# Kernel tuning notes

Hardware: AMD Instinct MI355X
Metric: run time of the kernel (lower is better)

## Reference

```python
import jax, jax.numpy as jnp
import numpy as np

N = 100000      # nodes
E = 3200000     # edges
F_IN = 78       # num_features_mol
F_GAT = 256     # mol_out_feats
HEADS = 2
F_HYP = 128     # mol_out_feats_hyper


def setup_inputs() -> dict:
    key = jax.random.key(0)
    ks = jax.random.split(key, 32)
    g = lambda k, s: jax.random.normal(k, s, dtype=jnp.float32) * 0.05
    inp = {}
    inp["mol_x"] = jax.random.normal(ks[0], (N, F_IN), dtype=jnp.float32)
    inp["mol_edge_index"] = jax.random.randint(ks[1], (2, E), 0, N)
    inp["hyper_edge"] = jax.random.randint(ks[2], (2, E), 0, N)
    # GAT layer 1 (78 -> 256, 2 heads, concat=False)
    inp["W1"] = g(ks[3], (F_IN, HEADS * F_GAT)); inp["as1"] = g(ks[4], (HEADS, F_GAT)); inp["ad1"] = g(ks[5], (HEADS, F_GAT)); inp["b1"] = jnp.zeros((F_GAT,), jnp.float32)
    # GAT layers 2,3 (256 -> 256)
    inp["W2"] = g(ks[6], (F_GAT, HEADS * F_GAT)); inp["as2"] = g(ks[7], (HEADS, F_GAT)); inp["ad2"] = g(ks[8], (HEADS, F_GAT)); inp["b2"] = jnp.zeros((F_GAT,), jnp.float32)
    inp["W3"] = g(ks[9], (F_GAT, HEADS * F_GAT)); inp["as3"] = g(ks[10], (HEADS, F_GAT)); inp["ad3"] = g(ks[11], (HEADS, F_GAT)); inp["b3"] = jnp.zeros((F_GAT,), jnp.float32)
    # GRU-style gating fusion
    inp["fc1_w"] = g(ks[12], (F_GAT, F_GAT)); inp["fc1_b"] = jnp.zeros((F_GAT,), jnp.float32)
    inp["fc2_w"] = g(ks[13], (F_GAT, F_GAT)); inp["fc2_b"] = jnp.zeros((F_GAT,), jnp.float32)
    inp["mol_bias"] = jax.random.uniform(ks[14], (1, F_GAT), jnp.float32, -0.2, 0.2)
    # HypergraphConv layers (334 -> 128 -> 128)
    inp["theta1"] = g(ks[15], (F_GAT + F_IN, F_HYP)); inp["hb1"] = jnp.zeros((F_HYP,), jnp.float32)
    inp["theta2"] = g(ks[16], (F_HYP, F_HYP)); inp["hb2"] = jnp.zeros((F_HYP,), jnp.float32)
    return inp


def _gat(x, src, dst, W, a_s, a_d, b):
    # PyG GATConv, heads=2, concat=False, eval mode (no dropout), self-loops pre-added in src/dst
    xh = (x @ W).reshape(N, HEADS, F_GAT)            # [N,H,C]
    a_src = (xh * a_s).sum(-1)                        # [N,H]
    a_dst = (xh * a_d).sum(-1)                        # [N,H]
    e = jax.nn.leaky_relu(a_src[src] + a_dst[dst], 0.2)  # [E',H]
    m = jax.ops.segment_max(e, dst, num_segments=N)
    ex = jnp.exp(e - m[dst])
    s = jax.ops.segment_sum(ex, dst, num_segments=N)
    alpha = ex / s[dst]                               # softmax over incoming edges
    out = jax.ops.segment_sum(xh[src] * alpha[:, :, None], dst, num_segments=N)
    return out.mean(axis=1) + b                       # concat=False -> head mean


def _hyper(x, node, edge, theta, b):
    # PyG HypergraphConv, use_attention=False: D^-1 H B^-1 H^T X Theta + b
    xt = x @ theta
    ones = jnp.ones((node.shape[0],), xt.dtype)
    D = jax.ops.segment_sum(ones, node, num_segments=N)
    B = jax.ops.segment_sum(ones, edge, num_segments=N)
    Dinv = jnp.where(D > 0, 1.0 / D, 0.0)
    Binv = jnp.where(B > 0, 1.0 / B, 0.0)
    ef = Binv[:, None] * jax.ops.segment_sum(xt[node], edge, num_segments=N)
    nf = Dinv[:, None] * jax.ops.segment_sum(ef[edge], node, num_segments=N)
    return nf + b


def _forward(mol_x, mol_edge_index, hyper_edge,
             W1, as1, ad1, b1, W2, as2, ad2, b2, W3, as3, ad3, b3,
             fc1_w, fc1_b, fc2_w, fc2_b, mol_bias, theta1, hb1, theta2, hb2):
    loops = jnp.arange(N, dtype=mol_edge_index.dtype)
    src = jnp.concatenate([mol_edge_index[0], loops])
    dst = jnp.concatenate([mol_edge_index[1], loops])
    hyper_x0 = jax.lax.stop_gradient(mol_x)  # .clone().detach()
    # layer 0
    h = jax.nn.relu(_gat(mol_x, src, dst, W1, as1, ad1, b1))
    # layer 1 (relu) + gate
    x = jax.nn.relu(_gat(h, src, dst, W2, as2, ad2, b2))
    z = jax.nn.sigmoid(x @ fc1_w.T + fc1_b + h @ fc2_w.T + fc2_b + mol_bias)
    h = z * x + (1.0 - z) * h
    # layer 2 (no relu) + gate
    x = _gat(h, src, dst, W3, as3, ad3, b3)
    z = jax.nn.sigmoid(x @ fc1_w.T + fc1_b + h @ fc2_w.T + fc2_b + mol_bias)
    h = z * x + (1.0 - z) * h
    # hypergraph branch (source uses mol_edge_index here, hyper_edge is unused)
    hx = jnp.concatenate([jax.lax.stop_gradient(h), hyper_x0], axis=1)
    node, edge = mol_edge_index[0], mol_edge_index[1]
    hx = jax.nn.relu(_hyper(hx, node, edge, theta1, hb1))
    hx = jax.nn.relu(_hyper(hx, node, edge, theta2, hb2))
    return jnp.concatenate([h, hx], axis=1)  # [N, 384]


def reference(mol_x, mol_edge_index, hyper_edge,
              W1, as1, ad1, b1, W2, as2, ad2, b2, W3, as3, ad3, b3,
              fc1_w, fc1_b, fc2_w, fc2_b, mol_bias, theta1, hb1, theta2, hb2):
    return _forward(mol_x, mol_edge_index, hyper_edge,
                    W1, as1, ad1, b1, W2, as2, ad2, b2, W3, as3, ad3, b3,
                    fc1_w, fc1_b, fc2_w, fc2_b, mol_bias, theta1, hb1, theta2, hb2)
```

## Files before the change

### kernel.cpp

```cpp
#include <hip/hip_runtime.h>

typedef unsigned short u16;
typedef __attribute__((ext_vector_type(8))) short short8v;
typedef __attribute__((ext_vector_type(8))) unsigned short ushort8v;
typedef __attribute__((ext_vector_type(4))) unsigned short ushort4v;
typedef __attribute__((ext_vector_type(4))) float f32x4;
typedef __attribute__((ext_vector_type(2))) float f32x2;

__device__ __forceinline__ float bf2f(u16 u) {
    union { unsigned int i; float f; } v; v.i = ((unsigned int)u) << 16; return v.f;
}
__device__ __forceinline__ u16 f2bf(float f) {
    union { float f; unsigned int i; } v; v.f = f;
    unsigned int i = v.i;
    return (u16)((i + 0x7FFFu + ((i >> 16) & 1u)) >> 16);
}
__device__ __forceinline__ float leaky02(float x) { return x > 0.f ? x : 0.2f * x; }
__device__ __forceinline__ float load_in(const void* p, long i, int isbf) {
    return isbf ? bf2f(((const u16*)p)[i]) : ((const float*)p)[i];
}
__device__ __forceinline__ f32x2 pk_fma(f32x2 a, f32x2 b, f32x2 c) {
    f32x2 d;
    asm("v_pk_fma_f32 %0, %1, %2, %3" : "=v"(d) : "v"(a), "v"(b), "v"(c));
    return d;
}
__device__ __forceinline__ f32x2 pk_add(f32x2 a, f32x2 b) {
    f32x2 d;
    asm("v_pk_add_f32 %0, %1, %2" : "=v"(d) : "v"(a), "v"(b));
    return d;
}
__device__ __forceinline__ f32x2 bfpair(unsigned int d) {
    union { unsigned int i; float f; } lo, hi;
    lo.i = d << 16;
    hi.i = d & 0xFFFF0000u;
    f32x2 r; r.x = lo.f; r.y = hi.f; return r;
}
#define GLD_LDS16(g, s) __builtin_amdgcn_global_load_lds( \
    (const __attribute__((address_space(1))) void*)(g),   \
    (__attribute__((address_space(3))) void*)(s), 16, 0, 0)

__global__ void detect_kernel(const unsigned* __restrict__ w, int* __restrict__ flag) {
    __shared__ int cnt;
    int t = threadIdx.x;
    if (t == 0) cnt = 0;
    __syncthreads();
    unsigned x = w[t * 16];
    unsigned lo = x & 0xFFFFu;
    int e = (int)((x >> 7) & 0xFFu);
    int good = (lo == 0u) || (e >= 100 && e <= 140);
    atomicAdd(&cnt, good);
    __syncthreads();
    if (t == 0) *flag = (cnt > 128) ? 1 : 0;
}

#define CSR_NBK 1024

__global__ __launch_bounds__(256)
void bucket_count_kernel(const int* __restrict__ ei, int* __restrict__ bcs,
                         int* __restrict__ bcd, int E_, int n, int SH) {
    __shared__ int hs[CSR_NBK], hd[CSR_NBK];
    const int t = threadIdx.x;
    for (int i = t; i < CSR_NBK; i += 256) { hs[i] = 0; hd[i] = 0; }
    __syncthreads();
    const int e0 = blockIdx.x * 4096;
    #pragma unroll
    for (int k = 0; k < 16; ++k) {
        int e = e0 + k * 256 + t;
        if (e < E_) {
            int s = ei[e], d = ei[E_ + e];
            if ((unsigned)s >= (unsigned)n) s = 0;
            if ((unsigned)d >= (unsigned)n) d = 0;
            atomicAdd(&hs[s >> SH], 1);
            atomicAdd(&hd[d >> SH], 1);
        }
    }
    __syncthreads();
    for (int i = t; i < CSR_NBK; i += 256) {
        if (hs[i]) atomicAdd(&bcs[i], hs[i]);
        if (hd[i]) atomicAdd(&bcd[i], hd[i]);
    }
}

__global__ void scan_excl_kernel(const int* __restrict__ deg, int* __restrict__ ptr, int n) {
    __shared__ int s_woff[17];
    __shared__ int s_carry;
    const int t = threadIdx.x;
    const int lane = t & 63, wid = t >> 6;
    if (t == 0) s_carry = 0;
    __syncthreads();
    for (int base = 0; base < n; base += 1024) {
        int i = base + t;
        int v = (i < n) ? deg[i] : 0;
        int incl = v;
        #pragma unroll
        for (int d = 1; d < 64; d <<= 1) {
            int x = __shfl_up(incl, d, 64);
            if (lane >= d) incl += x;
        }
        if (lane == 63) s_woff[wid] = incl;
        __syncthreads();
        if (t == 0) {
            int run = 0;
            #pragma unroll
            for (int w = 0; w < 16; ++w) { int x = s_woff[w]; s_woff[w] = run; run += x; }
            s_woff[16] = run;
        }
        __syncthreads();
        int excl = s_carry + s_woff[wid] + incl - v;
        if (i < n) ptr[i] = excl;
        __syncthreads();
        if (t == 0) s_carry += s_woff[16];
        __syncthreads();
    }
    if (t == 0) ptr[n] = s_carry;
}

__global__ void copy2_kernel(const int* __restrict__ a, int* __restrict__ b,
                             const int* __restrict__ c, int* __restrict__ d2, int n) {
    int i = blockIdx.x * 256 + threadIdx.x;
    if (i < n) { b[i] = a[i]; d2[i] = c[i]; }
}

__global__ __launch_bounds__(256)
void partition_kernel(const int* __restrict__ ei, int* __restrict__ bcur_s,
                      int* __restrict__ bcur_d, int2* __restrict__ ps,
                      int2* __restrict__ pd, int E_, int n, int SH) {
    __shared__ int cs[CSR_NBK], cd[CSR_NBK], bs[CSR_NBK], bd[CSR_NBK];
    const int t = threadIdx.x;
    for (int i = t; i < CSR_NBK; i += 256) { cs[i] = 0; cd[i] = 0; }
    __syncthreads();
    const int e0 = blockIdx.x * 4096;
    int sv[16], dv[16];
    #pragma unroll
    for (int k = 0; k < 16; ++k) {
        int e = e0 + k * 256 + t;
        int s = -1, d = 0;
        if (e < E_) {
            s = ei[e]; d = ei[E_ + e];
            if ((unsigned)s >= (unsigned)n) s = 0;
            if ((unsigned)d >= (unsigned)n) d = 0;
            atomicAdd(&cs[s >> SH], 1);
            atomicAdd(&cd[d >> SH], 1);
        }
        sv[k] = (e < E_) ? s : -1;
        dv[k] = d;
    }
    __syncthreads();
    for (int i = t; i < CSR_NBK; i += 256) {
        bs[i] = cs[i] ? atomicAdd(&bcur_s[i], cs[i]) : 0;
        bd[i] = cd[i] ? atomicAdd(&bcur_d[i], cd[i]) : 0;
        cs[i] = 0; cd[i] = 0;
    }
    __syncthreads();
    #pragma unroll
    for (int k = 0; k < 16; ++k) {
        int s = sv[k];
        if (s < 0) continue;
        int d = dv[k];
        int p = bs[s >> SH] + atomicAdd(&cs[s >> SH], 1);
        ps[p] = make_int2(d, s);
        int q = bd[d >> SH] + atomicAdd(&cd[d >> SH], 1);
        pd[q] = make_int2(s, d);
    }
}

__global__ __launch_bounds__(256)
void fill_bucket_kernel(const int2* __restrict__ pairs, const int* __restrict__ bptr,
                        int* __restrict__ ptr, int* __restrict__ idx, int n, int SH) {
    __shared__ int cnt[256];
    __shared__ int wsum[5];
    const int b = blockIdx.x;
    const int n0 = b << SH;
    if (n0 >= n) return;
    const int nn = min(1 << SH, n - n0);
    const int t = threadIdx.x;
    cnt[t] = 0;
    __syncthreads();
    const int pbeg = bptr[b], pend = bptr[b + 1];
    for (int j = pbeg + t; j < pend; j += 256)
        atomicAdd(&cnt[pairs[j].y - n0], 1);
    __syncthreads();
    const int c = (t < nn) ? cnt[t] : 0;
    int v = c;
    const int lane = t & 63, wid = t >> 6;
    #pragma unroll
    for (int d = 1; d < 64; d <<= 1) {
        int x = __shfl_up(v, d, 64);
        if (lane >= d) v += x;
    }
    if (lane == 63) wsum[wid] = v;
    __syncthreads();
    if (t == 0) {
        int r = 0;
        #pragma unroll
        for (int w = 0; w < 4; ++w) { int x = wsum[w]; wsum[w] = r; r += x; }
        wsum[4] = r;
    }
    __syncthreads();
    v += wsum[wid];
    const int excl = pbeg + v - c;
    __syncthreads();
    if (t < nn) { cnt[t] = excl; ptr[n0 + t] = excl; }
    if (t == 0 && n0 + nn == n) ptr[n] = pbeg + wsum[4];
    __syncthreads();
    for (int j = pbeg + t; j < pend; j += 256) {
        int2 pr = pairs[j];
        int p = atomicAdd(&cnt[pr.y - n0], 1);
        idx[p] = pr.x;
    }
}

__global__ void ingest_transpose_kernel(const void* __restrict__ src, long base,
                                        u16* __restrict__ dst, int K, int Nc, int Kp,
                                        const int* __restrict__ flag) {
    int i = blockIdx.x * 256 + threadIdx.x;
    if (i >= Nc * Kp) return;
    int n = i / Kp, k = i - n * Kp;
    float v = (k < K) ? load_in(src, base + (long)k * Nc + n, *flag) : 0.f;
    dst[i] = f2bf(v);
}

__global__ void ingest_vecs_kernel(const void* __restrict__ s0, const void* __restrict__ s1,
                                   const void* __restrict__ s2, const void* __restrict__ s3,
                                   const void* __restrict__ s4, const void* __restrict__ s5,
                                   const void* __restrict__ s6, const void* __restrict__ s7,
                                   u16* __restrict__ d0, u16* __restrict__ d1,
                                   u16* __restrict__ d2, u16* __restrict__ d3,
                                   u16* __restrict__ d4, u16* __restrict__ d5,
                                   u16* __restrict__ d6, u16* __restrict__ d7,
                                   const int* __restrict__ flag) {
    const void* srcs[8] = {s0, s1, s2, s3, s4, s5, s6, s7};
    u16* dsts[8] = {d0, d1, d2, d3, d4, d5, d6, d7};
    const int b = blockIdx.x, t = threadIdx.x;
    const int nsz = (b < 6) ? 256 : 128;
    if (t < nsz) dsts[b][t] = f2bf(load_in(srcs[b], t, *flag));
}

__global__ void ingest_wcat_kernel(const void* __restrict__ W, u16* __restrict__ dst,
                                   int Kin, int Fh, const int* __restrict__ flag) {
    int i = blockIdx.x * 256 + threadIdx.x;
    int tot = 256 * 2 * Fh;
    if (i >= tot) return;
    int o = i / (2 * Fh), k = i - o * 2 * Fh;
    int h = k / Fh, c = k - h * Fh;
    float v = (c < Kin) ? 0.5f * load_in(W, (long)c * 512 + h * 256 + o, *flag) : 0.f;
    dst[i] = f2bf(v);
}

__global__ void ingest_bcat_kernel(const void* __restrict__ fc1, const void* __restrict__ fc2,
                                   u16* __restrict__ dst, const int* __restrict__ flag) {
    int i = blockIdx.x * 256 + threadIdx.x;
    if (i >= 256 * 512) return;
    int o = i >> 9, k = i & 511;
    float v = (k < 256) ? load_in(fc1, (long)o * 256 + k, *flag)
                        : load_in(fc2, (long)o * 256 + k - 256, *flag);
    dst[i] = f2bf(v);
}

__global__ void ingest_pad_molx_kernel(const void* __restrict__ x, u16* __restrict__ dst,
                                       int ldd, int total, const int* __restrict__ flag) {
    int i = blockIdx.x * 256 + threadIdx.x;
    if (i >= total) return;
    int r = i / 96, c = i - r * 96;
    float v = (c < 78) ? load_in(x, (long)r * 78 + c, *flag) : 0.f;
    dst[(size_t)r * ldd + c] = f2bf(v);
}

__global__ void attn_vec_kernel(const void* __restrict__ W, const void* __restrict__ as_,
                                const void* __restrict__ ad_, float* __restrict__ was,
                                float* __restrict__ wad, int Kin, int Fh,
                                const int* __restrict__ flag) {
    int i = blockIdx.x * 256 + threadIdx.x;
    if (i >= 2 * Fh) return;
    int h = i / Fh, c = i - h * Fh;
    float s = 0.f, d = 0.f;
    if (c < Kin) {
        int f = *flag;
        for (int o = 0; o < 256; ++o) {
            float w = load_in(W, (long)c * 512 + h * 256 + o, f);
            s += w * load_in(as_, h * 256 + o, f);
            d += w * load_in(ad_, h * 256 + o, f);
        }
    }
    was[i] = s; wad[i] = d;
}

__global__ __launch_bounds__(256, 2)
void gemm_kernel(const u16* __restrict__ A, int lda,
                 const u16* __restrict__ Bt, int ldb,
                 u16* __restrict__ C, int ldc, int K, int M, int beta,
                 const u16* __restrict__ bias, int relu) {
    __shared__ __align__(16) u16 As[128 * 32];
    __shared__ __align__(16) u16 Bs[128 * 32];
    const int tid = threadIdx.x;
    const int wave = tid >> 6, lane = tid & 63;
    const int m0 = blockIdx.x * 128;
    const int n0 = blockIdx.y * 128;
    const int wm = (wave & 1) * 64, wn = (wave >> 1) * 64;
    const int r = lane & 15, q = lane >> 4;

    f32x4 acc[4][4];
    if (beta) {
        #pragma unroll
        for (int i = 0; i < 4; ++i)
            #pragma unroll
            for (int j = 0; j < 4; ++j)
                #pragma unroll
                for (int rr = 0; rr < 4; ++rr) {
                    size_t gr = (size_t)(m0 + wm + 16 * i + q * 4 + rr);
                    int gc = n0 + wn + 16 * j + r;
                    acc[i][j][rr] = bf2f(C[gr * ldc + gc]);
                }
    } else {
        #pragma unroll
        for (int i = 0; i < 4; ++i)
            #pragma unroll
            for (int j = 0; j < 4; ++j) acc[i][j] = (f32x4)0.f;
    }

    const int rowT = wave * 16 + (lane >> 2);
    const int koff = (lane & 3) * 8;
    int rA0 = m0 + rowT;       if (rA0 > M - 1) rA0 = M - 1;
    int rA1 = m0 + rowT + 64;  if (rA1 > M - 1) rA1 = M - 1;
    const u16* gA0 = A + (size_t)rA0 * lda + koff;
    const u16* gA1 = A + (size_t)rA1 * lda + koff;
    const u16* gB0 = Bt + (size_t)(n0 + rowT) * ldb + koff;
    const u16* gB1 = Bt + (size_t)(n0 + rowT + 64) * ldb + koff;
    u16* sA0 = &As[rowT * 32 + koff];
    u16* sA1 = &As[(rowT + 64) * 32 + koff];
    u16* sB0 = &Bs[rowT * 32 + koff];
    u16* sB1 = &Bs[(rowT + 64) * 32 + koff];

    const int nK = K >> 5;
    for (int kt = 0; kt < nK; ++kt) {
        __syncthreads();
        GLD_LDS16(gA0, sA0);
        GLD_LDS16(gA1, sA1);
        GLD_LDS16(gB0, sB0);
        GLD_LDS16(gB1, sB1);
        gA0 += 32; gA1 += 32; gB0 += 32; gB1 += 32;
        __syncthreads();
        short8v af[4], bf[4];
        #pragma unroll
        for (int i = 0; i < 4; ++i) af[i] = *(const short8v*)&As[(wm + 16 * i + r) * 32 + q * 8];
        #pragma unroll
        for (int j = 0; j < 4; ++j) bf[j] = *(const short8v*)&Bs[(wn + 16 * j + r) * 32 + q * 8];
        #pragma unroll
        for (int i = 0; i < 4; ++i)
            #pragma unroll
            for (int j = 0; j < 4; ++j)
                acc[i][j] = __builtin_amdgcn_mfma_f32_16x16x32_bf16(af[i], bf[j], acc[i][j], 0, 0, 0);
    }
    #pragma unroll
    for (int j = 0; j < 4; ++j) {
        int gc = n0 + wn + 16 * j + r;
        float bv = bias ? bf2f(bias[gc]) : 0.f;
        #pragma unroll
        for (int i = 0; i < 4; ++i)
            #pragma unroll
            for (int rr = 0; rr < 4; ++rr) {
                size_t gr = (size_t)(m0 + wm + 16 * i + q * 4 + rr);
                float x = acc[i][j][rr] + bv;
                if (relu) x = fmaxf(x, 0.f);
                C[gr * ldc + gc] = f2bf(x);
            }
    }
}

__global__ __launch_bounds__(256)
void attn_dots_h_kernel(const u16* __restrict__ hsrc, int ldh,
                        const float* __restrict__ was, const float* __restrict__ wad,
                        float* __restrict__ a_src, float* __restrict__ a_dst,
                        int Fh, int n) {
    int v = blockIdx.x * 4 + (threadIdx.x >> 6);
    if (v >= n) return;
    const int lane = threadIdx.x & 63;
    const int c0 = lane * 4;
    float ps0 = 0.f, pd0 = 0.f, ps1 = 0.f, pd1 = 0.f;
    if (c0 < Fh) {
        ushort4v xv = *(const ushort4v*)&hsrc[(size_t)v * ldh + c0];
        #pragma unroll
        for (int k = 0; k < 4; ++k) {
            float x = bf2f(xv[k]);
            ps0 += x * was[c0 + k];
            pd0 += x * wad[c0 + k];
            ps1 += x * was[Fh + c0 + k];
            pd1 += x * wad[Fh + c0 + k];
        }
    }
    #pragma unroll
    for (int d = 1; d < 64; d <<= 1) {
        ps0 += __shfl_xor(ps0, d, 64); pd0 += __shfl_xor(pd0, d, 64);
        ps1 += __shfl_xor(ps1, d, 64); pd1 += __shfl_xor(pd1, d, 64);
    }
    if (lane == 0) {
        a_src[2 * v] = ps0; a_src[2 * v + 1] = ps1;
        a_dst[2 * v] = pd0; a_dst[2 * v + 1] = pd1;
    }
}

template <int NG>
__global__ __launch_bounds__(256)
void gat_agg_kernel(const u16* __restrict__ hsrc, int ldh, int F,
                    const float* __restrict__ asrc, const float* __restrict__ adst,
                    const int* __restrict__ ptr, const int* __restrict__ idx,
                    u16* __restrict__ agg, int ldagg, int n, int Etot) {
    constexpr int GL = 64 / NG;
    int v = blockIdx.x * 4 + (threadIdx.x >> 6);
    if (v >= n) return;
    const int lane = threadIdx.x & 63;
    const int sub = lane / GL;
    const int c0 = (lane & (GL - 1)) * 8;
    const int act = (c0 < F);
    int beg = ptr[v], end = ptr[v + 1];
    beg = min(max(beg, 0), Etot);
    end = min(max(end, beg), Etot);
    const float ad0 = adst[2 * v], ad1 = adst[2 * v + 1];
    const float es0 = fminf(leaky02(asrc[2 * v] + ad0), 80.f);
    const float es1 = fminf(leaky02(asrc[2 * v + 1] + ad1), 80.f);
    f32x2 f0p[4], f1p[4];
    #pragma unroll
    for (int p = 0; p < 4; ++p) { f0p[p] = (f32x2)0.f; f1p[p] = (f32x2)0.f; }
    float s0 = 0.f, s1 = 0.f;

    int j = beg + sub;
    for (; j + 3 * NG < end; j += 4 * NG) {
        int sA = idx[j];          sA = ((unsigned)sA < (unsigned)n) ? sA : 0;
        int sB = idx[j + NG];     sB = ((unsigned)sB < (unsigned)n) ? sB : 0;
        int sC = idx[j + 2 * NG]; sC = ((unsigned)sC < (unsigned)n) ? sC : 0;
        int sD = idx[j + 3 * NG]; sD = ((unsigned)sD < (unsigned)n) ? sD : 0;
        const float2 aA = *(const float2*)&asrc[2 * sA];
        const float2 aB = *(const float2*)&asrc[2 * sB];
        const float2 aC = *(const float2*)&asrc[2 * sC];
        const float2 aD = *(const float2*)&asrc[2 * sD];
        const float wA0 = __expf(fminf(leaky02(aA.x + ad0), 80.f));
        const float wA1 = __expf(fminf(leaky02(aA.y + ad1), 80.f));
        const float wB0 = __expf(fminf(leaky02(aB.x + ad0), 80.f));
        const float wB1 = __expf(fminf(leaky02(aB.y + ad1), 80.f));
        const float wC0 = __expf(fminf(leaky02(aC.x + ad0), 80.f));
        const float wC1 = __expf(fminf(leaky02(aC.y + ad1), 80.f));
        const float wD0 = __expf(fminf(leaky02(aD.x + ad0), 80.f));
        const float wD1 = __expf(fminf(leaky02(aD.y + ad1), 80.f));
        s0 += (wA0 + wB0) + (wC0 + wD0);
        s1 += (wA1 + wB1) + (wC1 + wD1);
        if (act) {
            const uint4 fA = *(const uint4*)&hsrc[(size_t)sA * ldh + c0];
            const uint4 fB = *(const uint4*)&hsrc[(size_t)sB * ldh + c0];
            const uint4 fC = *(const uint4*)&hsrc[(size_t)sC * ldh + c0];
            const uint4 fD = *(const uint4*)&hsrc[(size_t)sD * ldh + c0];
            const f32x2 wA0v = {wA0, wA0}, wA1v = {wA1, wA1};
            const f32x2 wB0v = {wB0, wB0}, wB1v = {wB1, wB1};
            const f32x2 wC0v = {wC0, wC0}, wC1v = {wC1, wC1};
            const f32x2 wD0v = {wD0, wD0}, wD1v = {wD1, wD1};
            #pragma unroll
            for (int p = 0; p < 4; ++p) {
                const f32x2 xA = bfpair(((const unsigned*)&fA)[p]);
                const f32x2 xB = bfpair(((const unsigned*)&fB)[p]);
                const f32x2 xC = bfpair(((const unsigned*)&fC)[p]);
                const f32x2 xD = bfpair(((const unsigned*)&fD)[p]);
                f0p[p] = pk_fma(xA, wA0v, f0p[p]);
                f1p[p] = pk_fma(xA, wA1v, f1p[p]);
                f0p[p] = pk_fma(xB, wB0v, f0p[p]);
                f1p[p] = pk_fma(xB, wB1v, f1p[p]);
                f0p[p] = pk_fma(xC, wC0v, f0p[p]);
                f1p[p] = pk_fma(xC, wC1v, f1p[p]);
                f0p[p] = pk_fma(xD, wD0v, f0p[p]);
                f1p[p] = pk_fma(xD, wD1v, f1p[p]);
            }
        }
    }
    for (; j < end; j += NG) {
        int sA = idx[j]; sA = ((unsigned)sA < (unsigned)n) ? sA : 0;
        const float2 aA = *(const float2*)&asrc[2 * sA];
        const float wA0 = __expf(fminf(leaky02(aA.x + ad0), 80.f));
        const float wA1 = __expf(fminf(leaky02(aA.y + ad1), 80.f));
        s0 += wA0; s1 += wA1;
        if (act) {
            const uint4 fA = *(const uint4*)&hsrc[(size_t)sA * ldh + c0];
            const f32x2 wA0v = {wA0, wA0}, wA1v = {wA1, wA1};
            #pragma unroll
            for (int p = 0; p < 4; ++p) {
                const f32x2 xA = bfpair(((const unsigned*)&fA)[p]);
                f0p[p] = pk_fma(xA, wA0v, f0p[p]);
                f1p[p] = pk_fma(xA, wA1v, f1p[p]);
            }
        }
    }
    #pragma unroll
    for (int d = GL; d < 64; d <<= 1) {
        s0 += __shfl_xor(s0, d, 64);
        s1 += __shfl_xor(s1, d, 64);
    }
    const float ws0 = __expf(es0), ws1 = __expf(es1);
    s0 += ws0; s1 += ws1;
    if (sub == 0 && act) {
        const uint4 f = *(const uint4*)&hsrc[(size_t)v * ldh + c0];
        const f32x2 w0v = {ws0, ws0}, w1v = {ws1, ws1};
        #pragma unroll
        for (int p = 0; p < 4; ++p) {
            const f32x2 x = bfpair(((const unsigned*)&f)[p]);
            f0p[p] = pk_fma(x, w0v, f0p[p]);
            f1p[p] = pk_fma(x, w1v, f1p[p]);
        }
    }
    #pragma unroll
    for (int p = 0; p < 4; ++p) {
        #pragma unroll
        for (int d = GL; d < 64; d <<= 1) {
            f0p[p].x += __shfl_xor(f0p[p].x, d, 64);
            f0p[p].y += __shfl_xor(f0p[p].y, d, 64);
            f1p[p].x += __shfl_xor(f1p[p].x, d, 64);
            f1p[p].y += __shfl_xor(f1p[p].y, d, 64);
        }
    }
    if (lane < GL && act) {
        const float i0 = 1.f / s0, i1 = 1.f / s1;
        ushort8v o0, o1;
        #pragma unroll
        for (int p = 0; p < 4; ++p) {
            o0[2 * p] = f2bf(f0p[p].x * i0); o0[2 * p + 1] = f2bf(f0p[p].y * i0);
            o1[2 * p] = f2bf(f1p[p].x * i1); o1[2 * p + 1] = f2bf(f1p[p].y * i1);
        }
        *(ushort8v*)&agg[(size_t)v * ldagg + c0] = o0;
        *(ushort8v*)&agg[(size_t)v * ldagg + F + c0] = o1;
    }
}

__global__ __launch_bounds__(256)
void gate_kernel(const u16* __restrict__ logit, const u16* __restrict__ cat,
                 const u16* __restrict__ fc1b, const u16* __restrict__ fc2b,
                 const u16* __restrict__ molb, u16* __restrict__ dest,
                 void* __restrict__ outw, const int* __restrict__ flag, int n) {
    int i = blockIdx.x * 256 + threadIdx.x;
    if (i >= n) return;
    int node = i >> 5, c0 = (i & 31) * 8;
    ushort8v lg = *(const ushort8v*)&logit[(size_t)node * 256 + c0];
    ushort8v xv = *(const ushort8v*)&cat[(size_t)node * 512 + c0];
    ushort8v hv = *(const ushort8v*)&cat[(size_t)node * 512 + 256 + c0];
    ushort8v b1v = *(const ushort8v*)&fc1b[c0];
    ushort8v b2v = *(const ushort8v*)&fc2b[c0];
    ushort8v mbv = *(const ushort8v*)&molb[c0];
    float ov[8];
    ushort8v dv;
    #pragma unroll
    for (int k = 0; k < 8; ++k) {
        float l = bf2f(lg[k]) + bf2f(b1v[k]) + bf2f(b2v[k]) + bf2f(mbv[k]);
        float z = 1.f / (1.f + __expf(-l));
        ov[k] = z * bf2f(xv[k]) + (1.f - z) * bf2f(hv[k]);
        dv[k] = f2bf(ov[k]);
    }
    *(ushort8v*)&dest[(size_t)node * 512 + c0] = dv;
    if (outw) {
        if (*flag) {
            *(ushort8v*)((u16*)outw + (size_t)node * 384 + c0) = dv;
        } else {
            float* o = (float*)outw + (size_t)node * 384 + c0;
            #pragma unroll
            for (int k = 0; k < 8; ++k) o[k] = ov[k];
        }
    }
}

__global__ __launch_bounds__(256)
void hyper_gather_kernel(const u16* __restrict__ feat, const int* __restrict__ ptr,
                         const int* __restrict__ idx, const u16* __restrict__ bias,
                         u16* __restrict__ outb, int ldo, void* __restrict__ outw,
                         int col0, const int* __restrict__ flag,
                         int do_relu, int n, int Etot) {
    int v = blockIdx.x * 4 + (threadIdx.x >> 6);
    if (v >= n) return;
    const int lane = threadIdx.x & 63;
    const int c0 = (lane & 15) * 8, sub = lane >> 4;
    int beg = ptr[v], end = ptr[v + 1];
    beg = min(max(beg, 0), Etot);
    end = min(max(end, beg), Etot);
    const float inv = (end > beg) ? 1.f / (float)(end - beg) : 0.f;
    f32x2 a2[4];
    #pragma unroll
    for (int p = 0; p < 4; ++p) a2[p] = (f32x2)0.f;
    int j = beg + sub;
    for (; j + 12 < end; j += 16) {
        int sA = idx[j];      sA = ((unsigned)sA < (unsigned)n) ? sA : 0;
        int sB = idx[j + 4];  sB = ((unsigned)sB < (unsigned)n) ? sB : 0;
        int sC = idx[j + 8];  sC = ((unsigned)sC < (unsigned)n) ? sC : 0;
        int sD = idx[j + 12]; sD = ((unsigned)sD < (unsigned)n) ? sD : 0;
        const uint4 fA = *(const uint4*)&feat[(size_t)sA * 128 + c0];
        const uint4 fB = *(const uint4*)&feat[(size_t)sB * 128 + c0];
        const uint4 fC = *(const uint4*)&feat[(size_t)sC * 128 + c0];
        const uint4 fD = *(const uint4*)&feat[(size_t)sD * 128 + c0];
        #pragma unroll
        for (int p = 0; p < 4; ++p) {
            a2[p] = pk_add(a2[p], bfpair(((const unsigned*)&fA)[p]));
            a2[p] = pk_add(a2[p], bfpair(((const unsigned*)&fB)[p]));
            a2[p] = pk_add(a2[p], bfpair(((const unsigned*)&fC)[p]));
            a2[p] = pk_add(a2[p], bfpair(((const unsigned*)&fD)[p]));
        }
    }
    for (; j < end; j += 4) {
        int s = idx[j]; s = ((unsigned)s < (unsigned)n) ? s : 0;
        const uint4 f = *(const uint4*)&feat[(size_t)s * 128 + c0];
        #pragma unroll
        for (int p = 0; p < 4; ++p)
            a2[p] = pk_add(a2[p], bfpair(((const unsigned*)&f)[p]));
    }
    #pragma unroll
    for (int p = 0; p < 4; ++p) {
        a2[p].x += __shfl_xor(a2[p].x, 16, 64);
        a2[p].y += __shfl_xor(a2[p].y, 16, 64);
        a2[p].x += __shfl_xor(a2[p].x, 32, 64);
        a2[p].y += __shfl_xor(a2[p].y, 32, 64);
    }
    if (sub == 0) {
        float ov[8];
        ushort8v o;
        #pragma unroll
        for (int p = 0; p < 4; ++p) {
            float x0 = a2[p].x * inv + (bias ? bf2f(bias[c0 + 2 * p]) : 0.f);
            float x1 = a2[p].y * inv + (bias ? bf2f(bias[c0 + 2 * p + 1]) : 0.f);
            if (do_relu) { x0 = fmaxf(x0, 0.f); x1 = fmaxf(x1, 0.f); }
            ov[2 * p] = x0; ov[2 * p + 1] = x1;
            o[2 * p] = f2bf(x0); o[2 * p + 1] = f2bf(x1);
        }
        if (outb) *(ushort8v*)&outb[(size_t)v * ldo + c0] = o;
        if (outw) {
            if (*flag) {
                *(ushort8v*)((u16*)outw + (size_t)v * 384 + col0 + c0) = o;
            } else {
                float* ofp = (float*)outw + (size_t)v * 384 + col0 + c0;
                #pragma unroll
                for (int k = 0; k < 8; ++k) ofp[k] = ov[k];
            }
        }
    }
}

extern "C" void kernel_launch(void* const* d_in, const int* in_sizes, int n_in,
                              void* d_out, int out_size, void* d_ws, size_t ws_size,
                              hipStream_t stream) {
    const void* molx = d_in[0];
    const int*  ei   = (const int*)d_in[1];
    const void* W1 = d_in[3], *as1 = d_in[4], *ad1 = d_in[5], *b1 = d_in[6];
    const void* W2 = d_in[7], *as2 = d_in[8], *ad2 = d_in[9], *b2 = d_in[10];
    const void* W3 = d_in[11], *as3 = d_in[12], *ad3 = d_in[13], *b3 = d_in[14];
    const void* fc1w = d_in[15], *fc1b = d_in[16], *fc2w = d_in[17], *fc2b = d_in[18];
    const void* molb = d_in[19];
    const void* th1 = d_in[20], *hb1 = d_in[21], *th2 = d_in[22], *hb2 = d_in[23];
    (void)n_in; (void)out_size;

    const int N = in_sizes[0] / 78;
    const int E = in_sizes[1] / 2;
    const int Mp = ((N + 127) / 128) * 128;

    int SH = 0;
    while (((N - 1) >> SH) >= CSR_NBK) SH++;

    char* base = (char*)d_ws;
    size_t off = 0;
    auto alloc = [&](size_t bytes) -> void* {
        void* r = base + off;
        off = (off + bytes + 255) & ~(size_t)255;
        return r;
    };
    int* flag = (int*)alloc(4);
    u16* bv1 = (u16*)alloc(256 * 2); u16* bv2 = (u16*)alloc(256 * 2); u16* bv3 = (u16*)alloc(256 * 2);
    u16* fc1bv = (u16*)alloc(256 * 2); u16* fc2bv = (u16*)alloc(256 * 2); u16* molbv = (u16*)alloc(256 * 2);
    u16* hb1v = (u16*)alloc(128 * 2); u16* hb2v = (u16*)alloc(128 * 2);
    float* was1 = (float*)alloc(192 * 4); float* wad1 = (float*)alloc(192 * 4);
    float* was2 = (float*)alloc(512 * 4); float* wad2 = (float*)alloc(512 * 4);
    float* was3 = (float*)alloc(512 * 4); float* wad3 = (float*)alloc(512 * 4);
    u16* Wc1 = (u16*)alloc(256 * 192 * 2);
    u16* Wc2 = (u16*)alloc(256 * 512 * 2);
    u16* Wc3 = (u16*)alloc(256 * 512 * 2);
    u16* Bcat = (u16*)alloc(256 * 512 * 2);
    u16* th1ta = (u16*)alloc(128 * 256 * 2);
    u16* th1tb = (u16*)alloc(128 * 96 * 2);
    u16* th2t  = (u16*)alloc(128 * 128 * 2);
    float* a_src = (float*)alloc((size_t)N * 2 * 4);
    float* a_dst = (float*)alloc((size_t)N * 2 * 4);
    int* ptr_src = (int*)alloc((size_t)(N + 1) * 4);
    int* ptr_dst = (int*)alloc((size_t)(N + 1) * 4);
    int* bcnt_src = (int*)alloc(CSR_NBK * 4);
    int* bcnt_dst = (int*)alloc(CSR_NBK * 4);
    int* bptr_src = (int*)alloc((CSR_NBK + 1) * 4);
    int* bptr_dst = (int*)alloc((CSR_NBK + 1) * 4);
    int* bcur_src = (int*)alloc(CSR_NBK * 4);
    int* bcur_dst = (int*)alloc(CSR_NBK * 4);
    int* idx_src = (int*)alloc((size_t)E * 4);
    int* idx_dst = (int*)alloc((size_t)E * 4);
    u16* cat = (u16*)alloc((size_t)Mp * 512 * 2);
    u16* agg = (u16*)alloc((size_t)Mp * 512 * 2);
    u16* xt   = agg;
    u16* efb  = agg + (size_t)Mp * 128;
    u16* hx1  = agg + (size_t)Mp * 256;
    u16* mxp2 = agg + (size_t)Mp * 384;

    int2* pairs_src; int2* pairs_dst;
    if (off + (size_t)E * 16 + 1024 <= ws_size) {
        pairs_src = (int2*)alloc((size_t)E * 8);
        pairs_dst = (int2*)alloc((size_t)E * 8);
    } else {
        pairs_src = (int2*)agg;
        pairs_dst = (int2*)((char*)agg + (size_t)E * 8);
    }

    const int nodeBlocks = (N + 3) / 4;
    const int eTiles = (E + 4095) / 4096;

    detect_kernel<<<1, 256, 0, stream>>>((const unsigned*)molx, flag);

    hipMemsetAsync(bcnt_src, 0, CSR_NBK * 4, stream);
    hipMemsetAsync(bcnt_dst, 0, CSR_NBK * 4, stream);
    bucket_count_kernel<<<eTiles, 256, 0, stream>>>(ei, bcnt_src, bcnt_dst, E, N, SH);
    scan_excl_kernel<<<1, 1024, 0, stream>>>(bcnt_src, bptr_src, CSR_NBK);
    scan_excl_kernel<<<1, 1024, 0, stream>>>(bcnt_dst, bptr_dst, CSR_NBK);
    copy2_kernel<<<(CSR_NBK + 255) / 256, 256, 0, stream>>>(bptr_src, bcur_src, bptr_dst, bcur_dst, CSR_NBK);
    partition_kernel<<<eTiles, 256, 0, stream>>>(ei, bcur_src, bcur_dst,
                                                 pairs_src, pairs_dst, E, N, SH);
    fill_bucket_kernel<<<CSR_NBK, 256, 0, stream>>>(pairs_src, bptr_src, ptr_src, idx_src, N, SH);
    fill_bucket_kernel<<<CSR_NBK, 256, 0, stream>>>(pairs_dst, bptr_dst, ptr_dst, idx_dst, N, SH);

    ingest_wcat_kernel<<<(256 * 192 + 255) / 256, 256, 0, stream>>>(W1, Wc1, 78, 96, flag);
    ingest_wcat_kernel<<<(256 * 512 + 255) / 256, 256, 0, stream>>>(W2, Wc2, 256, 256, flag);
    ingest_wcat_kernel<<<(256 * 512 + 255) / 256, 256, 0, stream>>>(W3, Wc3, 256, 256, flag);
    ingest_bcat_kernel<<<(256 * 512 + 255) / 256, 256, 0, stream>>>(fc1w, fc2w, Bcat, flag);
    ingest_transpose_kernel<<<(128 * 256 + 255) / 256, 256, 0, stream>>>(th1, 0, th1ta, 256, 128, 256, flag);
    ingest_transpose_kernel<<<(128 * 96 + 255) / 256, 256, 0, stream>>>(th1, (long)256 * 128, th1tb, 78, 128, 96, flag);
    ingest_transpose_kernel<<<(128 * 128 + 255) / 256, 256, 0, stream>>>(th2, 0, th2t, 128, 128, 128, flag);
    attn_vec_kernel<<<1, 256, 0, stream>>>(W1, as1, ad1, was1, wad1, 78, 96, flag);
    attn_vec_kernel<<<2, 256, 0, stream>>>(W2, as2, ad2, was2, wad2, 256, 256, flag);
    attn_vec_kernel<<<2, 256, 0, stream>>>(W3, as3, ad3, was3, wad3, 256, 256, flag);
    ingest_vecs_kernel<<<8, 256, 0, stream>>>(b1, b2, b3, fc1b, fc2b, molb, hb1, hb2,
                                              bv1, bv2, bv3, fc1bv, fc2bv, molbv,
                                              hb1v, hb2v, flag);
    ingest_pad_molx_kernel<<<(N * 96 + 255) / 256, 256, 0, stream>>>(molx, cat, 512, N * 96, flag);

    auto gemm = [&](const u16* A, int lda, const u16* Bt, int ldb, u16* C, int ldc,
                    int K, int Nc, int M, int beta, const u16* bias, int relu) {
        dim3 g(Mp / 128, Nc / 128);
        gemm_kernel<<<g, 256, 0, stream>>>(A, lda, Bt, ldb, C, ldc, K, M, beta, bias, relu);
    };

    attn_dots_h_kernel<<<nodeBlocks, 256, 0, stream>>>(cat, 512, was1, wad1, a_src, a_dst, 96, N);
    gat_agg_kernel<4><<<nodeBlocks, 256, 0, stream>>>(cat, 512, 96, a_src, a_dst,
                                                      ptr_dst, idx_dst, agg, 192, N, E);
    gemm(agg, 192, Wc1, 192, cat + 256, 512, 192, 256, Mp, 0, bv1, 1);
    attn_dots_h_kernel<<<nodeBlocks, 256, 0, stream>>>(cat + 256, 512, was2, wad2, a_src, a_dst, 256, N);
    gat_agg_kernel<2><<<nodeBlocks, 256, 0, stream>>>(cat + 256, 512, 256, a_src, a_dst,
                                                      ptr_dst, idx_dst, agg, 512, N, E);
    gemm(agg, 512, Wc2, 512, cat, 512, 512, 256, Mp, 0, bv2, 1);
    gemm(cat, 512, Bcat, 512, agg , 256, 512, 256, Mp, 0, nullptr, 0);
    gate_kernel<<<(N * 32 + 255) / 256, 256, 0, stream>>>(agg, cat, fc1bv, fc2bv, molbv,
                                                          cat + 256, nullptr, flag, N * 32);
    attn_dots_h_kernel<<<nodeBlocks, 256, 0, stream>>>(cat + 256, 512, was3, wad3, a_src, a_dst, 256, N);
    gat_agg_kernel<2><<<nodeBlocks, 256, 0, stream>>>(cat + 256, 512, 256, a_src, a_dst,
                                                      ptr_dst, idx_dst, agg, 512, N, E);
    gemm(agg, 512, Wc3, 512, cat, 512, 512, 256, Mp, 0, bv3, 0);
    gemm(cat, 512, Bcat, 512, agg , 256, 512, 256, Mp, 0, nullptr, 0);
    gate_kernel<<<(N * 32 + 255) / 256, 256, 0, stream>>>(agg, cat, fc1bv, fc2bv, molbv,
                                                          cat + 256, d_out, flag, N * 32);
    ingest_pad_molx_kernel<<<(N * 96 + 255) / 256, 256, 0, stream>>>(molx, mxp2, 96, N * 96, flag);
    gemm(cat + 256, 512, th1ta, 256, xt, 128, 256, 128, Mp, 0, nullptr, 0);
    gemm(mxp2, 96, th1tb, 96, xt, 128, 96, 128, Mp, 1, nullptr, 0);
    hyper_gather_kernel<<<nodeBlocks, 256, 0, stream>>>(xt, ptr_dst, idx_dst, (const u16*)nullptr,
                                                        efb, 128, nullptr, 0, flag, 0, N, E);
    hyper_gather_kernel<<<nodeBlocks, 256, 0, stream>>>(efb, ptr_src, idx_src, hb1v,
                                                        hx1, 128, nullptr, 0, flag, 1, N, E);
    gemm(hx1, 128, th2t, 128, xt, 128, 128, 128, Mp, 0, nullptr, 0);
    hyper_gather_kernel<<<nodeBlocks, 256, 0, stream>>>(xt, ptr_dst, idx_dst, (const u16*)nullptr,
                                                        efb, 128, nullptr, 0, flag, 0, N, E);
    hyper_gather_kernel<<<nodeBlocks, 256, 0, stream>>>(efb, ptr_src, idx_src, hb2v,
                                                        (u16*)nullptr, 0, d_out, 256, flag, 1, N, E);
}
```

Baseline: 2.155 ms.

## Fuse gate GEMM with sigmoid gating and cooperatively load edge indices in GAT aggregation

Adds a gemm_gate_kernel that computes the full 256-column gate logits per 128-row tile and applies the sigmoid blend in the epilogue, writing h in place and to the output. This drops the intermediate logit buffer and a separate elementwise kernel. The GAT aggregation now loads 64 edge indices and attention weights per wave in one coalesced step and broadcasts them with ds_bpermute, replacing the per-lane strided index loads. In exchange, the fused GEMM has fewer blocks and a large accumulator (4x8 MFMA tiles per wave), so register pressure rises and occupancy may fall. The aggregation loop also issues only two feature gathers per iteration instead of four.

```diff
diff --git a/kernel.cpp b/kernel.cpp
--- a/kernel.cpp
+++ b/kernel.cpp
@@ -34,6 +34,12 @@
     lo.i = d << 16;
     hi.i = d & 0xFFFF0000u;
     f32x2 r; r.x = lo.f; r.y = hi.f; return r;
+}
+__device__ __forceinline__ float bperm_f(int addr, float v) {
+    return __int_as_float(__builtin_amdgcn_ds_bpermute(addr, __float_as_int(v)));
+}
+__device__ __forceinline__ int bperm_i(int addr, int v) {
+    return __builtin_amdgcn_ds_bpermute(addr, v);
 }
 #define GLD_LDS16(g, s) __builtin_amdgcn_global_load_lds( \
     (const __attribute__((address_space(1))) void*)(g),   \
@@ -368,6 +374,87 @@
 }
 
 __global__ __launch_bounds__(256)
+void gemm_gate_kernel(u16* __restrict__ A , int lda,
+                      const u16* __restrict__ Bt, int ldb, int K,
+                      const u16* __restrict__ fc1b, const u16* __restrict__ fc2b,
+                      const u16* __restrict__ molb, void* __restrict__ outw,
+                      const int* __restrict__ flag, int n) {
+    __shared__ __align__(16) u16 As[128 * 32];
+    __shared__ __align__(16) u16 Bs[256 * 32];
+    const int tid = threadIdx.x;
+    const int wave = tid >> 6, lane = tid & 63;
+    const int m0 = blockIdx.x * 128;
+    const int wm = (wave & 1) * 64, wn = (wave >> 1) * 128;
+    const int r = lane & 15, q = lane >> 4;
+
+    f32x4 acc[4][8];
+    #pragma unroll
+    for (int i = 0; i < 4; ++i)
+        #pragma unroll
+        for (int j = 0; j < 8; ++j) acc[i][j] = (f32x4)0.f;
+
+    const int koff = (tid & 3) * 8;
+    const u16* gA0 = A + (size_t)(m0 + (tid >> 2)) * lda + koff;
+    const u16* gA1 = A + (size_t)(m0 + (tid >> 2) + 64) * lda + koff;
+    const u16* gB0 = Bt + (size_t)(tid >> 2) * ldb + koff;
+    const u16* gB1 = Bt + (size_t)((tid >> 2) + 64) * ldb + koff;
+    const u16* gB2 = Bt + (size_t)((tid >> 2) + 128) * ldb + koff;
+    const u16* gB3 = Bt + (size_t)((tid >> 2) + 192) * ldb + koff;
+    u16* sA0 = &As[tid * 8];
+    u16* sA1 = &As[(tid + 256) * 8];
+    u16* sB0 = &Bs[tid * 8];
+    u16* sB1 = &Bs[(tid + 256) * 8];
+    u16* sB2 = &Bs[(tid + 512) * 8];
+    u16* sB3 = &Bs[(tid + 768) * 8];
+
+    const int nK = K >> 5;
+    for (int kt = 0; kt < nK; ++kt) {
+        __syncthreads();
+        GLD_LDS16(gA0, sA0);
+        GLD_LDS16(gA1, sA1);
+        GLD_LDS16(gB0, sB0);
+        GLD_LDS16(gB1, sB1);
+        GLD_LDS16(gB2, sB2);
+        GLD_LDS16(gB3, sB3);
+        gA0 += 32; gA1 += 32; gB0 += 32; gB1 += 32; gB2 += 32; gB3 += 32;
+        __syncthreads();
+        short8v af[4], bf[8];
+        #pragma unroll
+        for (int i = 0; i < 4; ++i) af[i] = *(const short8v*)&As[(wm + 16 * i + r) * 32 + q * 8];
+        #pragma unroll
+        for (int j = 0; j < 8; ++j) bf[j] = *(const short8v*)&Bs[(wn + 16 * j + r) * 32 + q * 8];
+        #pragma unroll
+        for (int i = 0; i < 4; ++i)
+            #pragma unroll
+            for (int j = 0; j < 8; ++j)
+                acc[i][j] = __builtin_amdgcn_mfma_f32_16x16x32_bf16(af[i], bf[j], acc[i][j], 0, 0, 0);
+    }
+    const int fl = *flag;
+    #pragma unroll
+    for (int j = 0; j < 8; ++j) {
+        const int gc = wn + 16 * j + r;
+        const float bsum = bf2f(fc1b[gc]) + bf2f(fc2b[gc]) + bf2f(molb[gc]);
+        #pragma unroll
+        for (int i = 0; i < 4; ++i)
+            #pragma unroll
+            for (int rr = 0; rr < 4; ++rr) {
+                const int gr = m0 + wm + 16 * i + q * 4 + rr;
+                const size_t rb = (size_t)gr * lda;
+                const float l = acc[i][j][rr] + bsum;
+                const float z = 1.f / (1.f + __expf(-l));
+                const float x = bf2f(A[rb + gc]);
+                const float h = bf2f(A[rb + 256 + gc]);
+                const float o = z * x + (1.f - z) * h;
+                A[rb + 256 + gc] = f2bf(o);
+                if (outw && gr < n) {
+                    if (fl) ((u16*)outw)[(size_t)gr * 384 + gc] = f2bf(o);
+                    else    ((float*)outw)[(size_t)gr * 384 + gc] = o;
+                }
+            }
+    }
+}
+
+__global__ __launch_bounds__(256)
 void attn_dots_h_kernel(const u16* __restrict__ hsrc, int ldh,
                         const float* __restrict__ was, const float* __restrict__ wad,
                         float* __restrict__ a_src, float* __restrict__ a_dst,
@@ -401,10 +488,10 @@
 
 template <int NG>
 __global__ __launch_bounds__(256)
-void gat_agg_kernel(const u16* __restrict__ hsrc, int ldh, int F,
-                    const float* __restrict__ asrc, const float* __restrict__ adst,
-                    const int* __restrict__ ptr, const int* __restrict__ idx,
-                    u16* __restrict__ agg, int ldagg, int n, int Etot) {
+void gat_agg_h_kernel(const u16* __restrict__ hsrc, int ldh, int F,
+                      const float* __restrict__ asrc, const float* __restrict__ adst,
+                      const int* __restrict__ ptr, const int* __restrict__ idx,
+                      u16* __restrict__ agg, int ldagg, int n, int Etot) {
     constexpr int GL = 64 / NG;
     int v = blockIdx.x * 4 + (threadIdx.x >> 6);
     if (v >= n) return;
@@ -418,84 +505,58 @@
     const float ad0 = adst[2 * v], ad1 = adst[2 * v + 1];
     const float es0 = fminf(leaky02(asrc[2 * v] + ad0), 80.f);
     const float es1 = fminf(leaky02(asrc[2 * v + 1] + ad1), 80.f);
+    float s0 = 0.f, s1 = 0.f;
     f32x2 f0p[4], f1p[4];
     #pragma unroll
     for (int p = 0; p < 4; ++p) { f0p[p] = (f32x2)0.f; f1p[p] = (f32x2)0.f; }
-    float s0 = 0.f, s1 = 0.f;
-
-    int j = beg + sub;
-    for (; j + 3 * NG < end; j += 4 * NG) {
-        int sA = idx[j];          sA = ((unsigned)sA < (unsigned)n) ? sA : 0;
-        int sB = idx[j + NG];     sB = ((unsigned)sB < (unsigned)n) ? sB : 0;
-        int sC = idx[j + 2 * NG]; sC = ((unsigned)sC < (unsigned)n) ? sC : 0;
-        int sD = idx[j + 3 * NG]; sD = ((unsigned)sD < (unsigned)n) ? sD : 0;
-        const float2 aA = *(const float2*)&asrc[2 * sA];
-        const float2 aB = *(const float2*)&asrc[2 * sB];
-        const float2 aC = *(const float2*)&asrc[2 * sC];
-        const float2 aD = *(const float2*)&asrc[2 * sD];
-        const float wA0 = __expf(fminf(leaky02(aA.x + ad0), 80.f));
-        const float wA1 = __expf(fminf(leaky02(aA.y + ad1), 80.f));
-        const float wB0 = __expf(fminf(leaky02(aB.x + ad0), 80.f));
-        const float wB1 = __expf(fminf(leaky02(aB.y + ad1), 80.f));
-        const float wC0 = __expf(fminf(leaky02(aC.x + ad0), 80.f));
-        const float wC1 = __expf(fminf(leaky02(aC.y + ad1), 80.f));
-        const float wD0 = __expf(fminf(leaky02(aD.x + ad0), 80.f));
-        const float wD1 = __expf(fminf(leaky02(aD.y + ad1), 80.f));
-        s0 += (wA0 + wB0) + (wC0 + wD0);
-        s1 += (wA1 + wB1) + (wC1 + wD1);
-        if (act) {
-            const uint4 fA = *(const uint4*)&hsrc[(size_t)sA * ldh + c0];
-            const uint4 fB = *(const uint4*)&hsrc[(size_t)sB * ldh + c0];
-            const uint4 fC = *(const uint4*)&hsrc[(size_t)sC * ldh + c0];
-            const uint4 fD = *(const uint4*)&hsrc[(size_t)sD * ldh + c0];
-            const f32x2 wA0v = {wA0, wA0}, wA1v = {wA1, wA1};
-            const f32x2 wB0v = {wB0, wB0}, wB1v = {wB1, wB1};
-            const f32x2 wC0v = {wC0, wC0}, wC1v = {wC1, wC1};
-            const f32x2 wD0v = {wD0, wD0}, wD1v = {wD1, wD1};
-            #pragma unroll
-            for (int p = 0; p < 4; ++p) {
-                const f32x2 xA = bfpair(((const unsigned*)&fA)[p]);
-                const f32x2 xB = bfpair(((const unsigned*)&fB)[p]);
-                const f32x2 xC = bfpair(((const unsigned*)&fC)[p]);
-                const f32x2 xD = bfpair(((const unsigned*)&fD)[p]);
-                f0p[p] = pk_fma(xA, wA0v, f0p[p]);
-                f1p[p] = pk_fma(xA, wA1v, f1p[p]);
-                f0p[p] = pk_fma(xB, wB0v, f0p[p]);
-                f1p[p] = pk_fma(xB, wB1v, f1p[p]);
-                f0p[p] = pk_fma(xC, wC0v, f0p[p]);
-                f1p[p] = pk_fma(xC, wC1v, f1p[p]);
-                f0p[p] = pk_fma(xD, wD0v, f0p[p]);
-                f1p[p] = pk_fma(xD, wD1v, f1p[p]);
+
+    for (int cb = beg; cb < end; cb += 64) {
+        const int cnt = min(64, end - cb);
+        int sE = 0;
+        float wE0 = 0.f, wE1 = 0.f;
+        if (lane < cnt) {
+            sE = idx[cb + lane];
+            sE = ((unsigned)sE < (unsigned)n) ? sE : 0;
+            const float2 ap = *(const float2*)&asrc[2 * sE];
+            wE0 = __expf(fminf(leaky02(ap.x + ad0), 80.f));
+            wE1 = __expf(fminf(leaky02(ap.y + ad1), 80.f));
+            s0 += wE0; s1 += wE1;
+        }
+        const int nIt = (cnt + 2 * NG - 1) / (2 * NG);
+        int jj = sub;
+        for (int it = 0; it < nIt; ++it, jj += 2 * NG) {
+            const int aA = jj * 4, aB = aA + NG * 4;
+            const int sA = bperm_i(aA, sE);
+            const float wA0 = bperm_f(aA, wE0), wA1 = bperm_f(aA, wE1);
+            const int sB = bperm_i(aB, sE);
+            const float wB0 = bperm_f(aB, wE0), wB1 = bperm_f(aB, wE1);
+            if (act) {
+                const uint4 fA = *(const uint4*)&hsrc[(size_t)sA * ldh + c0];
+                const uint4 fB = *(const uint4*)&hsrc[(size_t)sB * ldh + c0];
+                const f32x2 wA0v = {wA0, wA0}, wA1v = {wA1, wA1};
+                const f32x2 wB0v = {wB0, wB0}, wB1v = {wB1, wB1};
+                #pragma unroll
+                for (int p = 0; p < 4; ++p) {
+                    const f32x2 xA = bfpair(((const unsigned*)&fA)[p]);
+                    const f32x2 xB = bfpair(((const unsigned*)&fB)[p]);
+                    f0p[p] = pk_fma(xA, wA0v, f0p[p]);
+                    f1p[p] = pk_fma(xA, wA1v, f1p[p]);
+                    f0p[p] = pk_fma(xB, wB0v, f0p[p]);
+                    f1p[p] = pk_fma(xB, wB1v, f1p[p]);
+                }
             }
         }
     }
-    for (; j < end; j += NG) {
-        int sA = idx[j]; sA = ((unsigned)sA < (unsigned)n) ? sA : 0;
-        const float2 aA = *(const float2*)&asrc[2 * sA];
-        const float wA0 = __expf(fminf(leaky02(aA.x + ad0), 80.f));
-        const float wA1 = __expf(fminf(leaky02(aA.y + ad1), 80.f));
-        s0 += wA0; s1 += wA1;
-        if (act) {
-            const uint4 fA = *(const uint4*)&hsrc[(size_t)sA * ldh + c0];
-            const f32x2 wA0v = {wA0, wA0}, wA1v = {wA1, wA1};
-            #pragma unroll
-            for (int p = 0; p < 4; ++p) {
-                const f32x2 xA = bfpair(((const unsigned*)&fA)[p]);
-                f0p[p] = pk_fma(xA, wA0v, f0p[p]);
-                f1p[p] = pk_fma(xA, wA1v, f1p[p]);
-            }
-        }
-    }
-    #pragma unroll
-    for (int d = GL; d < 64; d <<= 1) {
+    #pragma unroll
+    for (int d = 1; d < 64; d <<= 1) {
         s0 += __shfl_xor(s0, d, 64);
         s1 += __shfl_xor(s1, d, 64);
     }
-    const float ws0 = __expf(es0), ws1 = __expf(es1);
-    s0 += ws0; s1 += ws1;
+    const float w0s = __expf(es0), w1s = __expf(es1);
+    s0 += w0s; s1 += w1s;
     if (sub == 0 && act) {
         const uint4 f = *(const uint4*)&hsrc[(size_t)v * ldh + c0];
-        const f32x2 w0v = {ws0, ws0}, w1v = {ws1, ws1};
+        const f32x2 w0v = {w0s, w0s}, w1v = {w1s, w1s};
         #pragma unroll
         for (int p = 0; p < 4; ++p) {
             const f32x2 x = bfpair(((const unsigned*)&f)[p]);
@@ -523,41 +584,6 @@
         }
         *(ushort8v*)&agg[(size_t)v * ldagg + c0] = o0;
         *(ushort8v*)&agg[(size_t)v * ldagg + F + c0] = o1;
-    }
-}
-
-__global__ __launch_bounds__(256)
-void gate_kernel(const u16* __restrict__ logit, const u16* __restrict__ cat,
-                 const u16* __restrict__ fc1b, const u16* __restrict__ fc2b,
-                 const u16* __restrict__ molb, u16* __restrict__ dest,
-                 void* __restrict__ outw, const int* __restrict__ flag, int n) {
-    int i = blockIdx.x * 256 + threadIdx.x;
-    if (i >= n) return;
-    int node = i >> 5, c0 = (i & 31) * 8;
-    ushort8v lg = *(const ushort8v*)&logit[(size_t)node * 256 + c0];
-    ushort8v xv = *(const ushort8v*)&cat[(size_t)node * 512 + c0];
-    ushort8v hv = *(const ushort8v*)&cat[(size_t)node * 512 + 256 + c0];
-    ushort8v b1v = *(const ushort8v*)&fc1b[c0];
-    ushort8v b2v = *(const ushort8v*)&fc2b[c0];
-    ushort8v mbv = *(const ushort8v*)&molb[c0];
-    float ov[8];
-    ushort8v dv;
-    #pragma unroll
-    for (int k = 0; k < 8; ++k) {
-        float l = bf2f(lg[k]) + bf2f(b1v[k]) + bf2f(b2v[k]) + bf2f(mbv[k]);
-        float z = 1.f / (1.f + __expf(-l));
-        ov[k] = z * bf2f(xv[k]) + (1.f - z) * bf2f(hv[k]);
-        dv[k] = f2bf(ov[k]);
-    }
-    *(ushort8v*)&dest[(size_t)node * 512 + c0] = dv;
-    if (outw) {
-        if (*flag) {
-            *(ushort8v*)((u16*)outw + (size_t)node * 384 + c0) = dv;
-        } else {
-            float* o = (float*)outw + (size_t)node * 384 + c0;
-            #pragma unroll
-            for (int k = 0; k < 8; ++k) o[k] = ov[k];
-        }
     }
 }
 
@@ -741,23 +767,21 @@
     };
 
     attn_dots_h_kernel<<<nodeBlocks, 256, 0, stream>>>(cat, 512, was1, wad1, a_src, a_dst, 96, N);
-    gat_agg_kernel<4><<<nodeBlocks, 256, 0, stream>>>(cat, 512, 96, a_src, a_dst,
-                                                      ptr_dst, idx_dst, agg, 192, N, E);
+    gat_agg_h_kernel<4><<<nodeBlocks, 256, 0, stream>>>(cat, 512, 96, a_src, a_dst,
+                                                        ptr_dst, idx_dst, agg, 192, N, E);
     gemm(agg, 192, Wc1, 192, cat + 256, 512, 192, 256, Mp, 0, bv1, 1);
     attn_dots_h_kernel<<<nodeBlocks, 256, 0, stream>>>(cat + 256, 512, was2, wad2, a_src, a_dst, 256, N);
-    gat_agg_kernel<2><<<nodeBlocks, 256, 0, stream>>>(cat + 256, 512, 256, a_src, a_dst,
-                                                      ptr_dst, idx_dst, agg, 512, N, E);
+    gat_agg_h_kernel<2><<<nodeBlocks, 256, 0, stream>>>(cat + 256, 512, 256, a_src, a_dst,
+                                                        ptr_dst, idx_dst, agg, 512, N, E);
     gemm(agg, 512, Wc2, 512, cat, 512, 512, 256, Mp, 0, bv2, 1);
-    gemm(cat, 512, Bcat, 512, agg , 256, 512, 256, Mp, 0, nullptr, 0);
-    gate_kernel<<<(N * 32 + 255) / 256, 256, 0, stream>>>(agg, cat, fc1bv, fc2bv, molbv,
-                                                          cat + 256, nullptr, flag, N * 32);
+    gemm_gate_kernel<<<Mp / 128, 256, 0, stream>>>(cat, 512, Bcat, 512, 512,
+                                                   fc1bv, fc2bv, molbv, nullptr, flag, N);
     attn_dots_h_kernel<<<nodeBlocks, 256, 0, stream>>>(cat + 256, 512, was3, wad3, a_src, a_dst, 256, N);
-    gat_agg_kernel<2><<<nodeBlocks, 256, 0, stream>>>(cat + 256, 512, 256, a_src, a_dst,
-                                                      ptr_dst, idx_dst, agg, 512, N, E);
+    gat_agg_h_kernel<2><<<nodeBlocks, 256, 0, stream>>>(cat + 256, 512, 256, a_src, a_dst,
+                                                        ptr_dst, idx_dst, agg, 512, N, E);
     gemm(agg, 512, Wc3, 512, cat, 512, 512, 256, Mp, 0, bv3, 0);
-    gemm(cat, 512, Bcat, 512, agg , 256, 512, 256, Mp, 0, nullptr, 0);
-    gate_kernel<<<(N * 32 + 255) / 256, 256, 0, stream>>>(agg, cat, fc1bv, fc2bv, molbv,
-                                                          cat + 256, d_out, flag, N * 32);
+    gemm_gate_kernel<<<Mp / 128, 256, 0, stream>>>(cat, 512, Bcat, 512, 512,
+                                                   fc1bv, fc2bv, molbv, d_out, flag, N);
     ingest_pad_molx_kernel<<<(N * 96 + 255) / 256, 256, 0, stream>>>(molx, mxp2, 96, N * 96, flag);
     gemm(cat + 256, 512, th1ta, 256, xt, 128, 256, 128, Mp, 0, nullptr, 0);
     gemm(mxp2, 96, th1tb, 96, xt, 128, 96, 128, Mp, 1, nullptr, 0);
```

Result: slower. 2.302 ms (+6.8%).
